# Kernel optimization log

Measured on AMD Instinct MI355X. Metric: run time of the kernel, lower is better.

The kernel has to match this reference:

```python
import jax, jax.numpy as jnp
import numpy as np

NUM_RADII, NUM_THETA = 3, 16
RADIUS = 40.0
DT = 0.1
RELU_SHIFT = 0.2
B, N, NB, T_ENC, OTHER_CH = 4, 512, 512, 16, 3


def _rot_mats():
    # bin-center angles of the num_theta angular bins
    t = (jnp.arange(NUM_THETA, dtype=jnp.float32) + 0.5) * (2.0 * jnp.pi / NUM_THETA) - jnp.pi
    c, s = jnp.cos(t), jnp.sin(t)
    return jnp.stack([jnp.stack([c, -s], -1), jnp.stack([s, c], -1)], -2)  # [T,2,2]


def _steer_kernel(W):
    # W: [R,T,O,I,2,2]; equivariant steering K[r,t] = R(theta_t) W[r,t] R(theta_t)^T
    Rm = _rot_mats()
    K = jnp.einsum('tab,rtoibc,tdc->rtoiad', Rm, W, Rm)
    return K.reshape(NUM_RADII * NUM_THETA, W.shape[2], W.shape[3], 2, 2)  # [K,O,I,2,2]


def _equi_conv(src_pos, qry_pos, feats, mask, W):
    # src_pos [B,S,2], qry_pos [B,Q,2], feats [B,S,I,2] vector features, mask [B,Q,S]
    rel = src_pos[:, None, :, :] - qry_pos[:, :, None, :]          # [B,Q,S,2]
    d2 = jnp.sum(rel * rel, -1)
    dist = jnp.sqrt(d2 + 1e-9)
    theta = jnp.arctan2(rel[..., 1], rel[..., 0])
    rb = jnp.clip((dist / RADIUS * NUM_RADII).astype(jnp.int32), 0, NUM_RADII - 1)
    tb = jnp.mod(jnp.floor((theta + jnp.pi) / (2.0 * jnp.pi) * NUM_THETA).astype(jnp.int32), NUM_THETA)
    kidx = rb * NUM_THETA + tb                                     # [B,Q,S] polar bin id
    win = jnp.maximum(1.0 - d2 / (RADIUS * RADIUS), 0.0) ** 3      # smooth radial window
    w = win * mask
    H = jax.nn.one_hot(kidx, NUM_RADII * NUM_THETA, dtype=feats.dtype) * w[..., None]  # [B,Q,S,K]
    M = jnp.einsum('bqsk,bsiv->bqkiv', H, feats)                   # bin-accumulated neighbor features
    K = _steer_kernel(W)
    return jnp.einsum('bqkiv,koiuv->bqou', M, K)                   # [B,Q,O,2]


def _equi_linear(f, A, Bm):
    # rotation-equivariant linear on vector channels: (a*I + b*J) per (out,in)
    Jf = jnp.stack([-f[..., 1], f[..., 0]], -1)
    return jnp.einsum('oi,bniv->bnov', A, f) + jnp.einsum('oi,bniv->bnov', Bm, Jf)


def _forward(p0_enc, v0_enc, p0, v0, a, other_feats, box, box_feats, fluid_mask, box_mask,
             W_cf, W_co, A_df, B_df, layer_params):
    # update_pos_vel
    v1 = v0 + DT * a
    p1 = p0 + DT * (v0 + v1) * 0.5
    # forward(): feats = cat(other_feats, v0_enc) on channel dim -2
    feats = jnp.concatenate([other_feats, v0_enc], -2)
    # compute_correction
    fluid_feats = jnp.concatenate([v1[:, :, None, :], feats], -2)  # [B,N,20,2]
    out_conv_fluid = _equi_conv(p1, p1, fluid_feats, fluid_mask, W_cf)
    out_dense_fluid = _equi_linear(fluid_feats, A_df, B_df)
    out_conv_obst = _equi_conv(box, p1, box_feats[:, :, None, :], box_mask, W_co)
    output = jnp.concatenate([out_conv_obst, out_conv_fluid, out_dense_fluid], -2)  # [B,N,48,2]
    for (Wc, Ad, Bd) in layer_params:
        mags = (jnp.sum(output * output, -1) + 1e-6)[..., None]
        in_feats = output / mags * jax.nn.relu(mags - RELU_SHIFT)
        oc = _equi_conv(p1, p1, in_feats, fluid_mask, Wc)
        od = _equi_linear(in_feats, Ad, Bd)
        if od.shape[-2] == output.shape[-2]:
            output = oc + od + output
        else:
            output = oc + od
    corr = output / 128.0                                          # [B,N,1,2]
    # apply_correction
    p_corrected = p1 + corr[..., 0, :]
    v_corrected = (p_corrected - p0) / DT
    return p_corrected, v_corrected


def setup_inputs():
    key = jax.random.key(0)
    ks = jax.random.split(key, 32)
    d = {}
    d['p0_enc'] = jax.random.normal(ks[0], (B, N, T_ENC, 2), jnp.float32)
    d['v0_enc'] = jax.random.normal(ks[1], (B, N, T_ENC, 2), jnp.float32)
    d['p0'] = jax.random.uniform(ks[2], (B, N, 2), jnp.float32) * 100.0
    d['v0'] = jax.random.normal(ks[3], (B, N, 2), jnp.float32)
    d['a'] = jax.random.normal(ks[4], (B, N, 2), jnp.float32)
    d['other_feats'] = jax.random.normal(ks[5], (B, N, OTHER_CH, 2), jnp.float32)
    d['box'] = jax.random.uniform(ks[6], (B, NB, 2), jnp.float32) * 100.0
    d['box_feats'] = jax.random.normal(ks[7], (B, NB, 2), jnp.float32)
    d['fluid_mask'] = (jax.random.uniform(ks[8], (B, N, N)) < 0.5).astype(jnp.float32)
    d['box_mask'] = (jax.random.uniform(ks[9], (B, N, NB)) < 0.5).astype(jnp.float32)
    sc = 0.05
    d['W_cf'] = sc * jax.random.normal(ks[10], (NUM_RADII, NUM_THETA, 16, 20, 2, 2), jnp.float32)
    d['W_co'] = sc * jax.random.normal(ks[11], (NUM_RADII, NUM_THETA, 16, 1, 2, 2), jnp.float32)
    d['A_df'] = sc * jax.random.normal(ks[12], (16, 20), jnp.float32)
    d['B_df'] = sc * jax.random.normal(ks[13], (16, 20), jnp.float32)
    chans = [(32, 48), (32, 32), (32, 32), (1, 32)]
    for i, (o, ci) in enumerate(chans, start=1):
        d['W_c%d' % i] = sc * jax.random.normal(ks[13 + 3 * i], (NUM_RADII, NUM_THETA, o, ci, 2, 2), jnp.float32)
        d['A_d%d' % i] = sc * jax.random.normal(ks[14 + 3 * i], (o, ci), jnp.float32)
        d['B_d%d' % i] = sc * jax.random.normal(ks[15 + 3 * i], (o, ci), jnp.float32)
    return d


def reference(p0_enc, v0_enc, p0, v0, a, other_feats, box, box_feats, fluid_mask, box_mask,
              W_cf, W_co, A_df, B_df, W_c1, A_d1, B_d1, W_c2, A_d2, B_d2,
              W_c3, A_d3, B_d3, W_c4, A_d4, B_d4):
    layer_params = [(W_c1, A_d1, B_d1), (W_c2, A_d2, B_d2), (W_c3, A_d3, B_d3), (W_c4, A_d4, B_d4)]
    return _forward(p0_enc, v0_enc, p0, v0, a, other_feats, box, box_feats, fluid_mask, box_mask,
                    W_cf, W_co, A_df, B_df, layer_params)
```

## Files before the change

### kernel.cpp

```cpp
#include <hip/hip_runtime.h>
#include <cstdint>
#include <cstddef>

#define PI_F 3.14159265358979323846f

constexpr int BB = 4, NN = 512, BN = 2048, NBIN = 48;

typedef __attribute__((ext_vector_type(8))) short v8s;
typedef __attribute__((ext_vector_type(4))) float v4f;

__device__ __forceinline__ unsigned short f2bf(float f) {
  unsigned u = __float_as_uint(f);
  unsigned r = (u + 0x7FFFu + ((u >> 16) & 1u)) >> 16;
  return (unsigned short)r;
}
__device__ __forceinline__ float bf2f(unsigned short s) {
  return __uint_as_float(((unsigned)s) << 16);
}

__device__ __forceinline__ void steer_f32(const float* __restrict__ W, float* __restrict__ K2,
                                          int O, int I, int Ipad, int idx, int total) {
  if (idx >= total) return;
  int i = idx % Ipad;
  int o = (idx / Ipad) % O;
  int k = idx / (Ipad * O);
  int CTc = O * 2;
  size_t r0 = (size_t)((k*Ipad + i)*2 + 0) * CTc + o*2;
  size_t r1 = r0 + CTc;
  if (i >= I) { K2[r0]=0.f; K2[r0+1]=0.f; K2[r1]=0.f; K2[r1+1]=0.f; return; }
  int tt = k % 16;
  float ang = (tt + 0.5f) * (2.0f * PI_F / 16.0f) - PI_F;
  float ct = cosf(ang), st = sinf(ang);
  const float* Wp = W + ((size_t)(k*O + o)*I + i) * 4;
  float w00 = Wp[0], w01 = Wp[1], w10 = Wp[2], w11 = Wp[3];
  float rw00 = ct*w00 - st*w10, rw01 = ct*w01 - st*w11;
  float rw10 = st*w00 + ct*w10, rw11 = st*w01 + ct*w11;
  K2[r0 + 0] = rw00*ct - rw01*st;
  K2[r0 + 1] = rw10*ct - rw11*st;
  K2[r1 + 0] = rw00*st + rw01*ct;
  K2[r1 + 1] = rw10*st + rw11*ct;
}

__device__ __forceinline__ void steer_bf16T(const float* __restrict__ W,
                                            unsigned short* __restrict__ K2T,
                                            int O, int I, int Ipad, int Kd,
                                            int idx, int total) {
  if (idx >= total) return;
  int i = idx % Ipad;
  int o = (idx / Ipad) % O;
  int k = idx / (Ipad * O);
  size_t c0 = (size_t)(o*2 + 0) * Kd + (k*Ipad + i)*2;
  size_t c1 = (size_t)(o*2 + 1) * Kd + (k*Ipad + i)*2;
  if (i >= I) { K2T[c0]=0; K2T[c0+1]=0; K2T[c1]=0; K2T[c1+1]=0; return; }
  int tt = k % 16;
  float ang = (tt + 0.5f) * (2.0f * PI_F / 16.0f) - PI_F;
  float ct = cosf(ang), st = sinf(ang);
  const float* Wp = W + ((size_t)(k*O + o)*I + i) * 4;
  float w00 = Wp[0], w01 = Wp[1], w10 = Wp[2], w11 = Wp[3];
  float rw00 = ct*w00 - st*w10, rw01 = ct*w01 - st*w11;
  float rw10 = st*w00 + ct*w10, rw11 = st*w01 + ct*w11;
  K2T[c0 + 0] = f2bf(rw00*ct - rw01*st);
  K2T[c0 + 1] = f2bf(rw00*st + rw01*ct);
  K2T[c1 + 0] = f2bf(rw10*ct - rw11*st);
  K2T[c1 + 1] = f2bf(rw10*st + rw11*ct);
}

__global__ __launch_bounds__(256) void setup_kernel(
    const float* __restrict__ p0, const float* __restrict__ v0,
    const float* __restrict__ a, const float* __restrict__ other,
    const float* __restrict__ v0enc, float* __restrict__ p1, float* __restrict__ F0,
    const float* Wcf, unsigned short* K2CF, const float* Wco, float* K2CO,
    const float* Wc1, unsigned short* K2C1, const float* Wc2, unsigned short* K2C2,
    const float* Wc3, unsigned short* K2C3, const float* Wc4, float* K2C4) {
  int blk = blockIdx.x;
  int t = threadIdx.x;
  if (blk < 8) {
    int n = blk * 256 + t;
    float p0x = p0[n*2], p0y = p0[n*2+1];
    float v0x = v0[n*2], v0y = v0[n*2+1];
    float ax = a[n*2],  ay = a[n*2+1];
    float v1x = v0x + 0.1f*ax, v1y = v0y + 0.1f*ay;
    p1[n*2]   = p0x + 0.1f*(v0x+v1x)*0.5f;
    p1[n*2+1] = p0y + 0.1f*(v0y+v1y)*0.5f;
    float* F = F0 + (size_t)n*48;
    F[0] = v1x; F[1] = v1y;
    for (int c = 0; c < 3; ++c) {
      F[2+c*2]   = other[(n*3+c)*2];
      F[2+c*2+1] = other[(n*3+c)*2+1];
    }
    for (int c = 0; c < 16; ++c) {
      F[8+c*2]   = v0enc[(n*16+c)*2];
      F[8+c*2+1] = v0enc[(n*16+c)*2+1];
    }
    for (int c = 40; c < 48; ++c) F[c] = 0.0f;
  } else if (blk < 80)  steer_bf16T(Wcf, K2CF, 16, 20, 24, 2304, (blk-8)*256 + t, 18432);
  else if (blk < 83)  steer_f32(Wco, K2CO, 16, 1, 1,   (blk-80)*256 + t, 768);
  else if (blk < 371) steer_bf16T(Wc1, K2C1, 32, 48, 48, 4608, (blk-83)*256 + t, 73728);
  else if (blk < 563) steer_bf16T(Wc2, K2C2, 32, 32, 32, 3072, (blk-371)*256 + t, 49152);
  else if (blk < 755) steer_bf16T(Wc3, K2C3, 32, 32, 32, 3072, (blk-563)*256 + t, 49152);
  else                steer_f32(Wc4, K2C4, 1, 32, 32,  (blk-755)*256 + t, 1536);
}

__global__ __launch_bounds__(256) void pairs_all(const float* __restrict__ qry,
                                                 const float* __restrict__ srcF,
                                                 const float* __restrict__ maskF,
                                                 float* __restrict__ wlF, int* __restrict__ plF,
                                                 int* __restrict__ cntF,
                                                 const float* __restrict__ srcO,
                                                 const float* __restrict__ maskO,
                                                 float* __restrict__ wlO, int* __restrict__ plO,
                                                 int* __restrict__ cntO) {
  __shared__ int hist[4][48];
  __shared__ int bstart[4][48];
  __shared__ int runc[4][48];
  bool isBox = blockIdx.x >= 512;
  int qblk = isBox ? (blockIdx.x - 512) : blockIdx.x;
  const float* src = isBox ? srcO : srcF;
  const float* mask = isBox ? maskO : maskF;
  float* wlist = isBox ? wlO : wlF;
  int* plist = isBox ? plO : plF;
  int* cnt = isBox ? cntO : cntF;

  int wv = threadIdx.x >> 6;
  int lane = threadIdx.x & 63;
  int q = qblk * 4 + wv;
  int b = q >> 9;
  float qx = qry[q*2], qy = qry[q*2+1];
  const float* sb = src + b*1024;
  const float* mb = mask + (size_t)q*512;
  float* wl = wlist + (size_t)q*512;
  int* pl = plist + (size_t)q*512;

  if (lane < 48) { hist[wv][lane] = 0; runc[wv][lane] = 0; }

  float wreg[8]; int kreg[8];
  unsigned char predreg[8];
  for (int ch = 0; ch < 8; ++ch) {
    int s = ch*64 + lane;
    float sx = sb[s*2], sy = sb[s*2+1];
    float rx = sx - qx, ry = sy - qy;
    float d2 = rx*rx + ry*ry;
    float m = mb[s];
    float wi = fmaxf(1.0f - d2 / 1600.0f, 0.0f);
    float w = wi*wi*wi*m;
    bool pred = w > 0.0f;
    int k = 63;
    if (pred) {
      float dist = sqrtf(d2 + 1e-9f);
      float theta = atan2f(ry, rx);
      int rb = (int)(dist / 40.0f * 3.0f);
      rb = rb > 2 ? 2 : rb;
      float u = (theta + PI_F) / (2.0f * PI_F) * 16.0f;
      int tb = ((int)floorf(u)) & 15;
      k = rb*16 + tb;
      atomicAdd(&hist[wv][k], 1);
    }
    wreg[ch] = w; kreg[ch] = k; predreg[ch] = pred ? 1 : 0;
  }
  int cntv = (lane < 48) ? hist[wv][lane] : 0;
  int sc = cntv;
  #pragma unroll
  for (int off = 1; off < 64; off <<= 1) {
    int o = __shfl_up(sc, off);
    if (lane >= off) sc += o;
  }
  if (lane < 48) bstart[wv][lane] = sc - cntv;
  if (lane == 47) cnt[q] = sc;

  for (int ch = 0; ch < 8; ++ch) {
    bool pred = predreg[ch] != 0;
    int k = kreg[ch];
    float w = wreg[ch];
    unsigned long long mEq = __ballot(pred);
    #pragma unroll
    for (int bit = 0; bit < 6; ++bit) {
      unsigned long long mbm = __ballot((k >> bit) & 1);
      mEq &= ((k >> bit) & 1) ? mbm : ~mbm;
    }
    int rank = __popcll(mEq & ((1ull<<lane)-1ull));
    int total = __popcll(mEq);
    if (pred) {
      int bs = bstart[wv][k];
      int rc = runc[wv][k];
      int pos = bs + rc + rank;
      int s = ch*64 + lane;
      wl[pos] = w;
      pl[pos] = (s<<6) | k;
      if (rank == total - 1) runc[wv][k] = rc + total;
    }
  }
}

__device__ __forceinline__ int find_split(const int* __restrict__ pls, int nnz) {
  if (nnz <= 0) return 0;
  int kmid = pls[nnz >> 1] & 63;
  int lo = nnz >> 1, hi = nnz;
  while (lo < hi) {
    int m2 = (lo + hi) >> 1;
    if ((pls[m2] & 63) > kmid) hi = m2; else lo = m2 + 1;
  }
  return lo;
}

template<int C2>
__device__ __forceinline__ void accum_range(float* __restrict__ M, int sw, int c,
    int jbeg, int jend,
    const float* __restrict__ wls, const int* __restrict__ pls,
    const float* __restrict__ fb) {
  int len = jend - jbeg;
  if (len <= 0) return;
  const float* wp = wls + jbeg;
  const int* pp = pls + jbeg;
  constexpr int W = 16;
  float wA[W], fA[W]; int kA[W];
  #pragma unroll
  for (int j = 0; j < W; ++j) {
    bool v = j < len;
    float wv = v ? wp[j] : 0.0f;
    int p = v ? pp[j] : 0;
    wA[j] = wv; kA[j] = v ? (p & 63) : NBIN;
    fA[j] = fb[(p >> 6) * C2];
  }
  int kcur = -1;
  float acc = 0.0f;
  for (int base = 0; base < len; base += W) {
    float wB[W], fB[W]; int kB[W];
    if (base + W < len) {
      #pragma unroll
      for (int j = 0; j < W; ++j) {
        int idx = base + W + j;
        bool v = idx < len;
        float wv = v ? wp[idx] : 0.0f;
        int p = v ? pp[idx] : 0;
        wB[j] = wv; kB[j] = v ? (p & 63) : NBIN;
        fB[j] = fb[(size_t)(p >> 6) * C2];
      }
    }
    asm volatile("" ::: "memory");
    #pragma unroll
    for (int j = 0; j < W; ++j) {
      acc = (kA[j] == kcur ? acc : 0.0f) + wA[j] * fA[j];
      kcur = kA[j];
      M[(kcur * C2 + c) ^ sw] = acc;
    }
    #pragma unroll
    for (int j = 0; j < W; ++j) { wA[j] = wB[j]; kA[j] = kB[j]; fA[j] = fB[j]; }
  }
}

template<int QB, int TPB>
__device__ __forceinline__ void stage_lists(int q0, const int* __restrict__ csh,
    const float* __restrict__ wlist, const int* __restrict__ plist,
    float* __restrict__ wsh, int* __restrict__ psh) {
  const int t = threadIdx.x;
  for (int i = t; i < QB*128; i += TPB) {
    int qs = i >> 7, j = i & 127;
    if (j*4 < csh[qs]) {
      ((float4*)(wsh + qs*512))[j] = ((const float4*)(wlist + (size_t)(q0+qs)*512))[j];
      ((int4*)(psh + qs*512))[j]   = ((const int4*)(plist + (size_t)(q0+qs)*512))[j];
    }
  }
}

template<int C2, int QB, int TPB>
__global__ __launch_bounds__(TPB, 1) void accum4(const float* __restrict__ wlist,
                                                 const int* __restrict__ plist,
                                                 const int* __restrict__ cnt,
                                                 const float* __restrict__ feats,
                                                 unsigned short* __restrict__ Mout) {
  constexpr int Kd = NBIN * C2;
  constexpr int KdP = Kd + C2;
  static_assert(TPB == 2 * QB * C2, "TPB must equal 2*QB*C2");
  __shared__ float Ml[QB * KdP];
  __shared__ float wsh[QB*512];
  __shared__ int   psh[QB*512];
  __shared__ int   csh[QB];
  const int t = threadIdx.x;
  const int q0 = blockIdx.x * QB;
  for (int i = t; i < QB*KdP; i += TPB) Ml[i] = 0.0f;
  if (t < QB) csh[t] = (q0 + t < BN) ? cnt[q0 + t] : 0;
  __syncthreads();
  stage_lists<QB, TPB>(q0, csh, wlist, plist, wsh, psh);
  __syncthreads();
  {
    const int ql = t / (2*C2);
    const int rem = t % (2*C2);
    const int half = rem / C2, c = rem % C2;
    const int q = q0 + ql;
    const int nnz = csh[ql];
    const int js = find_split(psh + ql*512, nnz);
    accum_range<C2>(Ml + ql*KdP, 0, c, half ? js : 0, half ? nnz : js,
                    wsh + ql*512, psh + ql*512,
                    feats + (size_t)(q >> 9)*512*C2 + c);
  }
  __syncthreads();
  for (int i = t; i < QB*(Kd/2); i += TPB) {
    int ql = i / (Kd/2), off = i % (Kd/2);
    float2 v = ((const float2*)(Ml + ql*KdP))[off];
    ((unsigned*)(Mout + (size_t)(q0+ql)*Kd))[off] =
        (unsigned)f2bf(v.x) | ((unsigned)f2bf(v.y) << 16);
  }
}

template<int CT>
__global__ __launch_bounds__(256) void gemm_mfma(const unsigned short* __restrict__ A,
                                                 const unsigned short* __restrict__ B,
                                                 float* __restrict__ G, int Kd, int kn) {
  const int lane = threadIdx.x & 63;
  const int w = threadIdx.x >> 6;
  const int mblk = blockIdx.x;
  const int ks = blockIdx.y * 4 + w;
  const int k0 = ks * kn;
  const int m = lane & 15, quad = lane >> 4;
  constexpr int NT = CT / 16;
  const unsigned short* Ar0 = A + (size_t)(mblk*32 + m) * Kd + k0 + quad*8;
  const unsigned short* Ar1 = Ar0 + (size_t)16 * Kd;
  const unsigned short* Bp[NT];
  #pragma unroll
  for (int nt = 0; nt < NT; ++nt)
    Bp[nt] = B + (size_t)(nt*16 + m) * Kd + k0 + quad*8;
  v4f acc[2][NT];
  #pragma unroll
  for (int mt = 0; mt < 2; ++mt)
    for (int nt = 0; nt < NT; ++nt)
      acc[mt][nt] = (v4f){0.0f, 0.0f, 0.0f, 0.0f};
  for (int kt = 0; kt < kn; kt += 32) {
    v8s a0 = *(const v8s*)(Ar0 + kt);
    v8s a1 = *(const v8s*)(Ar1 + kt);
    #pragma unroll
    for (int nt = 0; nt < NT; ++nt) {
      v8s bv = *(const v8s*)(Bp[nt] + kt);
      acc[0][nt] = __builtin_amdgcn_mfma_f32_16x16x32_bf16(a0, bv, acc[0][nt], 0, 0, 0);
      acc[1][nt] = __builtin_amdgcn_mfma_f32_16x16x32_bf16(a1, bv, acc[1][nt], 0, 0, 0);
    }
  }
  float* Gb = G + ((size_t)ks * BN + mblk*32) * CT;
  #pragma unroll
  for (int mt = 0; mt < 2; ++mt)
    for (int nt = 0; nt < NT; ++nt)
      for (int r = 0; r < 4; ++r)
        Gb[(mt*16 + quad*4 + r) * CT + nt*16 + m] = acc[mt][nt][r];
}

__global__ void epilogueL(const float* __restrict__ Gp, int SPLIT,
                          const float* __restrict__ inPrev, int I,
                          const float* __restrict__ Ad, const float* __restrict__ Bd,
                          const float* __restrict__ prevOut, int doRes,
                          float* __restrict__ outCur, float* __restrict__ inNext) {
  int idx = blockIdx.x * blockDim.x + threadIdx.x;
  if (idx >= BN*32) return;
  int o = idx % 32, q = idx / 32;
  float x = 0.0f, y = 0.0f;
  for (int sp = 0; sp < SPLIT; ++sp) {
    size_t base = ((size_t)sp*BN + q)*64 + o*2;
    x += Gp[base]; y += Gp[base+1];
  }
  const float* f = inPrev + (size_t)q * I * 2;
  for (int i = 0; i < I; ++i) {
    float fx = f[i*2], fy = f[i*2+1];
    float Av = Ad[o*I+i], Bv = Bd[o*I+i];
    x += Av*fx - Bv*fy;
    y += Av*fy + Bv*fx;
  }
  if (doRes) {
    x += prevOut[(size_t)idx*2];
    y += prevOut[(size_t)idx*2+1];
  }
  outCur[(size_t)idx*2]   = x;
  outCur[(size_t)idx*2+1] = y;
  float m = x*x + y*y + 1e-6f;
  float sc = fmaxf(m - 0.2f, 0.0f) / m;
  inNext[(size_t)idx*2]   = x * sc;
  inNext[(size_t)idx*2+1] = y * sc;
}

__global__ __launch_bounds__(512, 1) void fused_s0(
    const float* __restrict__ wlF, const int* __restrict__ plF, const int* __restrict__ cntF,
    const float* __restrict__ F0, const unsigned short* __restrict__ K2CF,
    const float* __restrict__ wlO, const int* __restrict__ plO, const int* __restrict__ cntO,
    const float* __restrict__ boxf, const float* __restrict__ K2CO,
    const float* __restrict__ Adf, const float* __restrict__ Bdf,
    float* __restrict__ in1) {
  constexpr int QB = 4;
  constexpr int Kd = 2304;
  constexpr int KdP = 2352;
  constexpr int NWv = 8;
  constexpr int KW = Kd / NWv;
  __shared__ float Ml[QB * KdP];
  __shared__ float Mo[QB * 98];
  __shared__ float red[NWv][QB * 32];
  __shared__ float wshF[QB*512];
  __shared__ int   pshF[QB*512];
  __shared__ float wshO[QB*512];
  __shared__ int   pshO[QB*512];
  __shared__ int cshF[QB];
  __shared__ int cshO[QB];
  const int t = threadIdx.x;
  const int q0 = blockIdx.x * QB;
  for (int i = t; i < QB*KdP; i += 512) Ml[i] = 0.0f;
  for (int i = t; i < QB*98; i += 512) Mo[i] = 0.0f;
  if (t < QB) cshF[t] = cntF[q0 + t];
  else if (t < 2*QB) cshO[t-QB] = cntO[q0 + t - QB];
  __syncthreads();
  for (int i = t; i < 2*QB*128; i += 512) {
    int half = i >> 9;
    int qs = (i >> 7) & (QB-1), j = i & 127;
    if (half == 0) {
      if (j*4 < cshF[qs]) {
        ((float4*)(wshF + qs*512))[j] = ((const float4*)(wlF + (size_t)(q0+qs)*512))[j];
        ((int4*)(pshF + qs*512))[j]   = ((const int4*)(plF + (size_t)(q0+qs)*512))[j];
      }
    } else {
      if (j*4 < cshO[qs]) {
        ((float4*)(wshO + qs*512))[j] = ((const float4*)(wlO + (size_t)(q0+qs)*512))[j];
        ((int4*)(pshO + qs*512))[j]   = ((const int4*)(plO + (size_t)(q0+qs)*512))[j];
      }
    }
  }
  __syncthreads();
  if (t < 384) {
    const int ql = t / 96, rem = t % 96;
    const int half = rem / 48, c = rem % 48;
    const int q = q0 + ql;
    const int nnz = cshF[ql];
    const int js = find_split(pshF + ql*512, nnz);
    accum_range<48>(Ml + ql*KdP, ql << 2, c, half ? js : 0, half ? nnz : js,
                    wshF + ql*512, pshF + ql*512,
                    F0 + (size_t)(q >> 9)*512*48 + c);
  } else if (t < 400) {
    const int idx = t - 384;
    const int ql = idx >> 2, half = (idx >> 1) & 1, c = idx & 1;
    const int q = q0 + ql;
    const int nnz = cshO[ql];
    const int js = find_split(pshO + ql*512, nnz);
    accum_range<2>(Mo + ql*98, 0, c, half ? js : 0, half ? nnz : js,
                   wshO + ql*512, pshO + ql*512,
                   boxf + (size_t)(q >> 9)*1024 + c);
  }
  __syncthreads();
  {
    const int lane = t & 63, w = t >> 6;
    const int m = lane & 15, quad = lane >> 4;
    const int ar = m & 3;
    const int sw = ar << 2;
    const float* Abase = Ml + ar * KdP;
    const int kb = w * KW + quad * 8;
    const unsigned short* Bb0 = K2CF + (size_t)m * Kd + kb;
    const unsigned short* Bb1 = K2CF + (size_t)(16 + m) * Kd + kb;
    v4f acc[2];
    acc[0] = (v4f){0,0,0,0}; acc[1] = (v4f){0,0,0,0};
    float4 a0c = *(const float4*)(Abase + (kb ^ sw));
    float4 a1c = *(const float4*)(Abase + ((kb + 4) ^ sw));
    v8s b0c = *(const v8s*)(Bb0);
    v8s b1c = *(const v8s*)(Bb1);
    for (int kt = 0; kt < KW; kt += 32) {
      float4 a0n, a1n; v8s b0n, b1n;
      if (kt + 32 < KW) {
        const int jn = kb + kt + 32;
        a0n = *(const float4*)(Abase + (jn ^ sw));
        a1n = *(const float4*)(Abase + ((jn + 4) ^ sw));
        b0n = *(const v8s*)(Bb0 + kt + 32);
        b1n = *(const v8s*)(Bb1 + kt + 32);
      }
      v8s av;
      av[0]=(short)f2bf(a0c.x); av[1]=(short)f2bf(a0c.y); av[2]=(short)f2bf(a0c.z); av[3]=(short)f2bf(a0c.w);
      av[4]=(short)f2bf(a1c.x); av[5]=(short)f2bf(a1c.y); av[6]=(short)f2bf(a1c.z); av[7]=(short)f2bf(a1c.w);
      acc[0] = __builtin_amdgcn_mfma_f32_16x16x32_bf16(av, b0c, acc[0], 0, 0, 0);
      acc[1] = __builtin_amdgcn_mfma_f32_16x16x32_bf16(av, b1c, acc[1], 0, 0, 0);
      a0c = a0n; a1c = a1n; b0c = b0n; b1c = b1n;
    }
    if (quad == 0) {
      #pragma unroll
      for (int nt = 0; nt < 2; ++nt)
        #pragma unroll
        for (int r = 0; r < 4; ++r)
          red[w][r*32 + nt*16 + m] = acc[nt][r];
    }
  }
  __syncthreads();
  if (t < 192) {
    const int ql = t / 48, ch = t % 48;
    const int q = q0 + ql;
    float x = 0.0f, y = 0.0f;
    if (ch < 16) {
      const float* Mq = Mo + ql*98;
      for (int j = 0; j < 96; ++j) {
        float mv = Mq[j];
        x += mv * K2CO[j*32 + ch*2];
        y += mv * K2CO[j*32 + ch*2 + 1];
      }
    } else if (ch < 32) {
      int o = ch - 16;
      #pragma unroll
      for (int w2 = 0; w2 < NWv; ++w2) {
        x += red[w2][ql*32 + o*2];
        y += red[w2][ql*32 + o*2 + 1];
      }
    } else {
      int o = ch - 32;
      const float* f = F0 + (size_t)q*48;
      for (int i = 0; i < 20; ++i) {
        float fx = f[i*2], fy = f[i*2+1];
        float Av = Adf[o*20+i], Bv = Bdf[o*20+i];
        x += Av*fx - Bv*fy;
        y += Av*fy + Bv*fx;
      }
    }
    float mm = x*x + y*y + 1e-6f;
    float sc = fmaxf(mm - 0.2f, 0.0f) / mm;
    size_t idx = (size_t)q*48 + ch;
    in1[idx*2]   = x * sc;
    in1[idx*2+1] = y * sc;
  }
}

template<int C2, int CT, int I, int QB>
__global__ __launch_bounds__(2*C2*QB, 1) void fused_layer(
    const float* __restrict__ wlist, const int* __restrict__ plist,
    const int* __restrict__ cnt, const float* __restrict__ feats,
    const unsigned short* __restrict__ K2T,
    const float* __restrict__ Ad, const float* __restrict__ Bd,
    const float* __restrict__ prevOut, int doRes,
    float* __restrict__ outCur, float* __restrict__ inNext) {
  constexpr int Kd = NBIN * C2;
  constexpr int KdP = Kd + C2;
  constexpr int TPB = 2 * C2 * QB;
  constexpr int NW = TPB / 64;
  constexpr int KW = Kd / NW;
  constexpr int NT = CT / 16;
  static_assert(KW % 32 == 0, "KW must be multiple of 32");
  __shared__ float Ml[QB * KdP];
  __shared__ float red[NW][QB * CT];
  __shared__ float wsh[QB*512];
  __shared__ int   psh[QB*512];
  __shared__ int csh[QB];
  const int t = threadIdx.x;
  const int q0 = blockIdx.x * QB;
  for (int i = t; i < QB*KdP; i += TPB) Ml[i] = 0.0f;
  if (t < QB) csh[t] = cnt[q0 + t];
  __syncthreads();
  stage_lists<QB, TPB>(q0, csh, wlist, plist, wsh, psh);
  __syncthreads();
  {
    const int ql = t / (2*C2);
    const int rem = t % (2*C2);
    const int half = rem / C2, c = rem % C2;
    const int q = q0 + ql;
    const int nnz = csh[ql];
    const int js = find_split(psh + ql*512, nnz);
    accum_range<C2>(Ml + ql*KdP, (ql & 3) << 2, c, half ? js : 0, half ? nnz : js,
                    wsh + ql*512, psh + ql*512,
                    feats + (size_t)(q >> 9)*512*C2 + c);
  }
  __syncthreads();
  const int lane = t & 63, w = t >> 6;
  const int m = lane & 15, quad = lane >> 4;
  const int ar = m & (QB-1);
  const int sw = ar << 2;
  const float* Abase = Ml + ar * KdP;
  const int kb = w * KW + quad * 8;
  const unsigned short* Bb[NT];
  #pragma unroll
  for (int nt = 0; nt < NT; ++nt)
    Bb[nt] = K2T + (size_t)(nt*16 + m) * Kd + kb;
  v4f acc[NT];
  #pragma unroll
  for (int nt = 0; nt < NT; ++nt) acc[nt] = (v4f){0,0,0,0};
  float4 a0c = *(const float4*)(Abase + (kb ^ sw));
  float4 a1c = *(const float4*)(Abase + ((kb + 4) ^ sw));
  v8s bc[NT];
  #pragma unroll
  for (int nt = 0; nt < NT; ++nt) bc[nt] = *(const v8s*)(Bb[nt]);
  for (int kt = 0; kt < KW; kt += 32) {
    float4 a0n, a1n; v8s bn[NT];
    if (kt + 32 < KW) {
      const int jn = kb + kt + 32;
      a0n = *(const float4*)(Abase + (jn ^ sw));
      a1n = *(const float4*)(Abase + ((jn + 4) ^ sw));
      #pragma unroll
      for (int nt = 0; nt < NT; ++nt) bn[nt] = *(const v8s*)(Bb[nt] + kt + 32);
    }
    v8s av;
    av[0]=(short)f2bf(a0c.x); av[1]=(short)f2bf(a0c.y); av[2]=(short)f2bf(a0c.z); av[3]=(short)f2bf(a0c.w);
    av[4]=(short)f2bf(a1c.x); av[5]=(short)f2bf(a1c.y); av[6]=(short)f2bf(a1c.z); av[7]=(short)f2bf(a1c.w);
    #pragma unroll
    for (int nt = 0; nt < NT; ++nt)
      acc[nt] = __builtin_amdgcn_mfma_f32_16x16x32_bf16(av, bc[nt], acc[nt], 0, 0, 0);
    a0c = a0n; a1c = a1n;
    #pragma unroll
    for (int nt = 0; nt < NT; ++nt) bc[nt] = bn[nt];
  }
  if (quad == 0) {
    #pragma unroll
    for (int nt = 0; nt < NT; ++nt)
      #pragma unroll
      for (int r = 0; r < QB; ++r)
        red[w][r*CT + nt*16 + m] = acc[nt][r];
  }
  __syncthreads();
  if (t < QB * (CT/2)) {
    const int o = t % (CT/2), ql = t / (CT/2);
    const int q = q0 + ql;
    float x = 0.0f, y = 0.0f;
    #pragma unroll
    for (int w2 = 0; w2 < NW; ++w2) {
      x += red[w2][ql*CT + o*2];
      y += red[w2][ql*CT + o*2 + 1];
    }
    const float* f = feats + (size_t)q * C2;
    for (int i = 0; i < I; ++i) {
      float fx = f[i*2], fy = f[i*2+1];
      float Av = Ad[o*I + i], Bv = Bd[o*I + i];
      x += Av*fx - Bv*fy;
      y += Av*fy + Bv*fx;
    }
    size_t idx = (size_t)q * (CT/2) + o;
    if (doRes) { x += prevOut[idx*2]; y += prevOut[idx*2+1]; }
    outCur[idx*2]   = x;
    outCur[idx*2+1] = y;
    float mm = x*x + y*y + 1e-6f;
    float sc = fmaxf(mm - 0.2f, 0.0f) / mm;
    inNext[idx*2]   = x * sc;
    inNext[idx*2+1] = y * sc;
  }
}

__global__ __launch_bounds__(512, 1) void fused_l4(
    const float* __restrict__ wl, const int* __restrict__ pl, const int* __restrict__ cnt,
    const float* __restrict__ in4, const float* __restrict__ K2C4,
    const float* __restrict__ Ad4, const float* __restrict__ Bd4,
    const float* __restrict__ p1, const float* __restrict__ p0,
    float* __restrict__ dout) {
  constexpr int QB = 4, Kd = 3072, KdP = 3136;
  __shared__ float Ml[QB * KdP];
  __shared__ float wsh[QB*512];
  __shared__ int   psh[QB*512];
  __shared__ int csh[QB];
  __shared__ float r4[QB][2][2];
  const int t = threadIdx.x;
  const int q0 = blockIdx.x * QB;
  for (int i = t; i < QB*KdP; i += 512) Ml[i] = 0.0f;
  if (t < QB) csh[t] = cnt[q0 + t];
  __syncthreads();
  stage_lists<QB, 512>(q0, csh, wl, pl, wsh, psh);
  __syncthreads();
  {
    const int ql = t / 128, rem = t % 128;
    const int half = rem / 64, c = rem % 64;
    const int q = q0 + ql;
    const int nnz = csh[ql];
    const int js = find_split(psh + ql*512, nnz);
    accum_range<64>(Ml + ql*KdP, (ql & 3) << 2, c, half ? js : 0, half ? nnz : js,
                    wsh + ql*512, psh + ql*512,
                    in4 + (size_t)(q >> 9)*512*64 + c);
  }
  __syncthreads();
  const int lane = t & 63, w = t >> 6;
  const int ql = w >> 1, kh = w & 1;
  const int q = q0 + ql;
  const int sw = ql << 2;
  const float* Mq = Ml + ql*KdP;
  float a0 = 0.0f, a1 = 0.0f;
  for (int j = kh*1536 + lane; j < kh*1536 + 1536; j += 64) {
    float av = Mq[j ^ sw];
    a0 += av * K2C4[j*2];
    a1 += av * K2C4[j*2+1];
  }
  if (kh == 0 && lane < 32) {
    float fx = in4[q*64 + lane*2], fy = in4[q*64 + lane*2 + 1];
    float Av = Ad4[lane], Bv = Bd4[lane];
    a0 += Av*fx - Bv*fy;
    a1 += Av*fy + Bv*fx;
  }
  for (int off = 32; off > 0; off >>= 1) {
    a0 += __shfl_down(a0, off);
    a1 += __shfl_down(a1, off);
  }
  if (lane == 0) { r4[ql][kh][0] = a0; r4[ql][kh][1] = a1; }
  __syncthreads();
  if (t < QB) {
    int qq = q0 + t;
    float s0 = r4[t][0][0] + r4[t][1][0];
    float s1 = r4[t][0][1] + r4[t][1][1];
    float px = p1[qq*2]   + s0/128.0f;
    float py = p1[qq*2+1] + s1/128.0f;
    dout[qq*2] = px; dout[qq*2+1] = py;
    dout[4096 + qq*2]   = (px - p0[qq*2]) / 0.1f;
    dout[4096 + qq*2+1] = (py - p0[qq*2+1]) / 0.1f;
  }
}

extern "C" void kernel_launch(void* const* d_in, const int* in_sizes, int n_in,
                              void* d_out, int out_size, void* d_ws, size_t ws_size,
                              hipStream_t stream) {
  (void)in_sizes; (void)n_in; (void)out_size; (void)ws_size;
  const float* v0_enc = (const float*)d_in[1];
  const float* p0     = (const float*)d_in[2];
  const float* v0     = (const float*)d_in[3];
  const float* a      = (const float*)d_in[4];
  const float* other  = (const float*)d_in[5];
  const float* box    = (const float*)d_in[6];
  const float* boxf   = (const float*)d_in[7];
  const float* fmask  = (const float*)d_in[8];
  const float* bmask  = (const float*)d_in[9];
  const float* Wcf = (const float*)d_in[10];
  const float* Wco = (const float*)d_in[11];
  const float* Adf = (const float*)d_in[12];
  const float* Bdf = (const float*)d_in[13];
  const float* Wc1 = (const float*)d_in[14];
  const float* Ad1 = (const float*)d_in[15];
  const float* Bd1 = (const float*)d_in[16];
  const float* Wc2 = (const float*)d_in[17];
  const float* Ad2 = (const float*)d_in[18];
  const float* Bd2 = (const float*)d_in[19];
  const float* Wc3 = (const float*)d_in[20];
  const float* Ad3 = (const float*)d_in[21];
  const float* Bd3 = (const float*)d_in[22];
  const float* Wc4 = (const float*)d_in[23];
  const float* Ad4 = (const float*)d_in[24];
  const float* Bd4 = (const float*)d_in[25];

  float* ws = (float*)d_ws;
  float* P1    = ws + 0;
  float* F0    = ws + 4096;
  unsigned short* K2CF = (unsigned short*)(ws + 102400);
  float* K2CO  = ws + 176128;
  unsigned short* K2C1 = (unsigned short*)(ws + 179200);
  unsigned short* K2C2 = (unsigned short*)(ws + 474112);
  unsigned short* K2C3 = (unsigned short*)(ws + 670720);
  float* K2C4  = ws + 867328;
  float* WFl   = ws + 873472;
  int*   PFl   = (int*)(ws + 1922048);
  int*   CNTF  = (int*)(ws + 2970624);
  int*   CNTO  = (int*)(ws + 2972672);
  float* IN1   = ws + 2974720;
  float* IN2   = ws + 3171328;
  float* IN3   = ws + 3302400;
  float* IN4   = ws + 3433472;
  float* OUTA  = ws + 3564544;
  float* OUTB  = ws + 3695616;
  float* GPART = ws + 4027392;
  unsigned short* MBUF = (unsigned short*)(ws + 6124544);
  float* WOl   = ws + 15561728;
  int*   POl   = (int*)(ws + 16610304);

  setup_kernel<<<761, 256, 0, stream>>>(p0, v0, a, other, v0_enc, P1, F0,
                                        Wcf, K2CF, Wco, K2CO, Wc1, K2C1,
                                        Wc2, K2C2, Wc3, K2C3, Wc4, K2C4);
  pairs_all<<<1024, 256, 0, stream>>>(P1, P1, fmask, WFl, PFl, CNTF,
                                      box, bmask, WOl, POl, CNTO);
  fused_s0<<<512, 512, 0, stream>>>(WFl, PFl, CNTF, F0, K2CF,
                                    WOl, POl, CNTO, boxf, K2CO, Adf, Bdf, IN1);
  accum4<96, 2, 384><<<1024, 384, 0, stream>>>(WFl, PFl, CNTF, IN1, MBUF);
  gemm_mfma<64><<<dim3(64, 4), 256, 0, stream>>>(MBUF, K2C1, GPART, 4608, 288);
  epilogueL<<<256, 256, 0, stream>>>(GPART, 16, IN1, 48, Ad1, Bd1, nullptr, 0, OUTA, IN2);
  fused_layer<64, 64, 32, 4><<<512, 512, 0, stream>>>(WFl, PFl, CNTF, IN2, K2C2,
                                                      Ad2, Bd2, OUTA, 1, OUTB, IN3);
  fused_layer<64, 64, 32, 4><<<512, 512, 0, stream>>>(WFl, PFl, CNTF, IN3, K2C3,
                                                      Ad3, Bd3, OUTB, 1, OUTA, IN4);
  fused_l4<<<512, 512, 0, stream>>>(WFl, PFl, CNTF, IN4, K2C4, Ad4, Bd4,
                                    P1, p0, (float*)d_out);
}
```

Baseline: 292.4 us.

## Merge setup and pair-building kernels; split neighbor accumulation into four segments

Setup and pair-list construction now run in one launch. The pair blocks recompute the updated positions inline instead of waiting on P1 from setup. The accum4 and fused_l4 kernels split each query's bin-sorted neighbor list into four segments instead of two, doubling threads per block, to get more parallelism in the accumulation. This removes one launch and a dependency, but recomputes positions redundantly and adds more segment boundaries, where threads working on the same bin may conflict.

```diff
diff --git a/kernel.cpp b/kernel.cpp
--- a/kernel.cpp
+++ b/kernel.cpp
@@ -65,15 +65,13 @@
   K2T[c1 + 1] = f2bf(rw10*st + rw11*ct);
 }
 
-__global__ __launch_bounds__(256) void setup_kernel(
+__device__ __forceinline__ void setup_body(int blk, int t,
     const float* __restrict__ p0, const float* __restrict__ v0,
     const float* __restrict__ a, const float* __restrict__ other,
     const float* __restrict__ v0enc, float* __restrict__ p1, float* __restrict__ F0,
     const float* Wcf, unsigned short* K2CF, const float* Wco, float* K2CO,
     const float* Wc1, unsigned short* K2C1, const float* Wc2, unsigned short* K2C2,
     const float* Wc3, unsigned short* K2C3, const float* Wc4, float* K2C4) {
-  int blk = blockIdx.x;
-  int t = threadIdx.x;
   if (blk < 8) {
     int n = blk * 256 + t;
     float p0x = p0[n*2], p0y = p0[n*2+1];
@@ -101,32 +99,42 @@
   else                steer_f32(Wc4, K2C4, 1, 32, 32,  (blk-755)*256 + t, 1536);
 }
 
-__global__ __launch_bounds__(256) void pairs_all(const float* __restrict__ qry,
-                                                 const float* __restrict__ srcF,
-                                                 const float* __restrict__ maskF,
-                                                 float* __restrict__ wlF, int* __restrict__ plF,
-                                                 int* __restrict__ cntF,
-                                                 const float* __restrict__ srcO,
-                                                 const float* __restrict__ maskO,
-                                                 float* __restrict__ wlO, int* __restrict__ plO,
-                                                 int* __restrict__ cntO) {
+__global__ __launch_bounds__(256) void setup_pairs(
+    const float* __restrict__ p0, const float* __restrict__ v0,
+    const float* __restrict__ a, const float* __restrict__ other,
+    const float* __restrict__ v0enc, float* __restrict__ P1, float* __restrict__ F0,
+    const float* Wcf, unsigned short* K2CF, const float* Wco, float* K2CO,
+    const float* Wc1, unsigned short* K2C1, const float* Wc2, unsigned short* K2C2,
+    const float* Wc3, unsigned short* K2C3, const float* Wc4, float* K2C4,
+    const float* __restrict__ maskF,
+    float* __restrict__ wlF, int* __restrict__ plF, int* __restrict__ cntF,
+    const float* __restrict__ box, const float* __restrict__ maskO,
+    float* __restrict__ wlO, int* __restrict__ plO, int* __restrict__ cntO) {
+  const int t = threadIdx.x;
+  if (blockIdx.x < 761) {
+    setup_body(blockIdx.x, t, p0, v0, a, other, v0enc, P1, F0,
+               Wcf, K2CF, Wco, K2CO, Wc1, K2C1, Wc2, K2C2, Wc3, K2C3, Wc4, K2C4);
+    return;
+  }
   __shared__ int hist[4][48];
   __shared__ int bstart[4][48];
   __shared__ int runc[4][48];
-  bool isBox = blockIdx.x >= 512;
-  int qblk = isBox ? (blockIdx.x - 512) : blockIdx.x;
-  const float* src = isBox ? srcO : srcF;
+  int pblk = blockIdx.x - 761;
+  bool isBox = pblk >= 512;
+  int qblk = isBox ? (pblk - 512) : pblk;
   const float* mask = isBox ? maskO : maskF;
   float* wlist = isBox ? wlO : wlF;
   int* plist = isBox ? plO : plF;
   int* cnt = isBox ? cntO : cntF;
 
-  int wv = threadIdx.x >> 6;
-  int lane = threadIdx.x & 63;
+  int wv = t >> 6;
+  int lane = t & 63;
   int q = qblk * 4 + wv;
   int b = q >> 9;
-  float qx = qry[q*2], qy = qry[q*2+1];
-  const float* sb = src + b*1024;
+  float qv1x = v0[q*2]   + 0.1f*a[q*2];
+  float qv1y = v0[q*2+1] + 0.1f*a[q*2+1];
+  float qx = p0[q*2]   + 0.1f*(v0[q*2]  +qv1x)*0.5f;
+  float qy = p0[q*2+1] + 0.1f*(v0[q*2+1]+qv1y)*0.5f;
   const float* mb = mask + (size_t)q*512;
   float* wl = wlist + (size_t)q*512;
   int* pl = plist + (size_t)q*512;
@@ -137,7 +145,16 @@
   unsigned char predreg[8];
   for (int ch = 0; ch < 8; ++ch) {
     int s = ch*64 + lane;
-    float sx = sb[s*2], sy = sb[s*2+1];
+    float sx, sy;
+    if (isBox) {
+      sx = box[(b*512+s)*2]; sy = box[(b*512+s)*2+1];
+    } else {
+      int n = b*512 + s;
+      float sv1x = v0[n*2]   + 0.1f*a[n*2];
+      float sv1y = v0[n*2+1] + 0.1f*a[n*2+1];
+      sx = p0[n*2]   + 0.1f*(v0[n*2]  +sv1x)*0.5f;
+      sy = p0[n*2+1] + 0.1f*(v0[n*2+1]+sv1y)*0.5f;
+    }
     float rx = sx - qx, ry = sy - qy;
     float d2 = rx*rx + ry*ry;
     float m = mb[s];
@@ -191,15 +208,18 @@
   }
 }
 
-__device__ __forceinline__ int find_split(const int* __restrict__ pls, int nnz) {
-  if (nnz <= 0) return 0;
-  int kmid = pls[nnz >> 1] & 63;
-  int lo = nnz >> 1, hi = nnz;
+__device__ __forceinline__ int find_split_at(const int* __restrict__ pls, int nnz, int target) {
+  if (target >= nnz) return nnz;
+  int kmid = pls[target] & 63;
+  int lo = target, hi = nnz;
   while (lo < hi) {
     int m2 = (lo + hi) >> 1;
     if ((pls[m2] & 63) > kmid) hi = m2; else lo = m2 + 1;
   }
   return lo;
+}
+__device__ __forceinline__ int find_split(const int* __restrict__ pls, int nnz) {
+  return find_split_at(pls, nnz, nnz >> 1);
 }
 
 template<int C2>
@@ -270,7 +290,7 @@
                                                  unsigned short* __restrict__ Mout) {
   constexpr int Kd = NBIN * C2;
   constexpr int KdP = Kd + C2;
-  static_assert(TPB == 2 * QB * C2, "TPB must equal 2*QB*C2");
+  static_assert(TPB == 4 * QB * C2, "TPB must equal 4*QB*C2");
   __shared__ float Ml[QB * KdP];
   __shared__ float wsh[QB*512];
   __shared__ int   psh[QB*512];
@@ -283,14 +303,16 @@
   stage_lists<QB, TPB>(q0, csh, wlist, plist, wsh, psh);
   __syncthreads();
   {
-    const int ql = t / (2*C2);
-    const int rem = t % (2*C2);
-    const int half = rem / C2, c = rem % C2;
+    const int ql = t / (4*C2);
+    const int rem = t % (4*C2);
+    const int seg = rem / C2, c = rem % C2;
     const int q = q0 + ql;
     const int nnz = csh[ql];
-    const int js = find_split(psh + ql*512, nnz);
-    accum_range<C2>(Ml + ql*KdP, 0, c, half ? js : 0, half ? nnz : js,
-                    wsh + ql*512, psh + ql*512,
+    const int* pls = psh + ql*512;
+    int b0 = (seg == 0) ? 0 : find_split_at(pls, nnz, (nnz*seg) >> 2);
+    int b1 = (seg == 3) ? nnz : find_split_at(pls, nnz, (nnz*(seg+1)) >> 2);
+    accum_range<C2>(Ml + ql*KdP, 0, c, b0, b1,
+                    wsh + ql*512, pls,
                     feats + (size_t)(q >> 9)*512*C2 + c);
   }
   __syncthreads();
@@ -625,7 +647,7 @@
   }
 }
 
-__global__ __launch_bounds__(512, 1) void fused_l4(
+__global__ __launch_bounds__(1024, 1) void fused_l4(
     const float* __restrict__ wl, const int* __restrict__ pl, const int* __restrict__ cnt,
     const float* __restrict__ in4, const float* __restrict__ K2C4,
     const float* __restrict__ Ad4, const float* __restrict__ Bd4,
@@ -636,37 +658,39 @@
   __shared__ float wsh[QB*512];
   __shared__ int   psh[QB*512];
   __shared__ int csh[QB];
-  __shared__ float r4[QB][2][2];
+  __shared__ float r4[QB][4][2];
   const int t = threadIdx.x;
   const int q0 = blockIdx.x * QB;
-  for (int i = t; i < QB*KdP; i += 512) Ml[i] = 0.0f;
+  for (int i = t; i < QB*KdP; i += 1024) Ml[i] = 0.0f;
   if (t < QB) csh[t] = cnt[q0 + t];
   __syncthreads();
-  stage_lists<QB, 512>(q0, csh, wl, pl, wsh, psh);
+  stage_lists<QB, 1024>(q0, csh, wl, pl, wsh, psh);
   __syncthreads();
   {
-    const int ql = t / 128, rem = t % 128;
-    const int half = rem / 64, c = rem % 64;
+    const int ql = t / 256, rem = t % 256;
+    const int seg = rem / 64, c = rem % 64;
     const int q = q0 + ql;
     const int nnz = csh[ql];
-    const int js = find_split(psh + ql*512, nnz);
-    accum_range<64>(Ml + ql*KdP, (ql & 3) << 2, c, half ? js : 0, half ? nnz : js,
-                    wsh + ql*512, psh + ql*512,
+    const int* pls = psh + ql*512;
+    int b0 = (seg == 0) ? 0 : find_split_at(pls, nnz, (nnz*seg) >> 2);
+    int b1 = (seg == 3) ? nnz : find_split_at(pls, nnz, (nnz*(seg+1)) >> 2);
+    accum_range<64>(Ml + ql*KdP, (ql & 3) << 2, c, b0, b1,
+                    wsh + ql*512, pls,
                     in4 + (size_t)(q >> 9)*512*64 + c);
   }
   __syncthreads();
   const int lane = t & 63, w = t >> 6;
-  const int ql = w >> 1, kh = w & 1;
+  const int ql = w >> 2, kq = w & 3;
   const int q = q0 + ql;
   const int sw = ql << 2;
   const float* Mq = Ml + ql*KdP;
   float a0 = 0.0f, a1 = 0.0f;
-  for (int j = kh*1536 + lane; j < kh*1536 + 1536; j += 64) {
+  for (int j = kq*768 + lane; j < kq*768 + 768; j += 64) {
     float av = Mq[j ^ sw];
     a0 += av * K2C4[j*2];
     a1 += av * K2C4[j*2+1];
   }
-  if (kh == 0 && lane < 32) {
+  if (kq == 0 && lane < 32) {
     float fx = in4[q*64 + lane*2], fy = in4[q*64 + lane*2 + 1];
     float Av = Ad4[lane], Bv = Bd4[lane];
     a0 += Av*fx - Bv*fy;
@@ -676,12 +700,12 @@
     a0 += __shfl_down(a0, off);
     a1 += __shfl_down(a1, off);
   }
-  if (lane == 0) { r4[ql][kh][0] = a0; r4[ql][kh][1] = a1; }
+  if (lane == 0) { r4[ql][kq][0] = a0; r4[ql][kq][1] = a1; }
   __syncthreads();
   if (t < QB) {
     int qq = q0 + t;
-    float s0 = r4[t][0][0] + r4[t][1][0];
-    float s1 = r4[t][0][1] + r4[t][1][1];
+    float s0 = r4[t][0][0] + r4[t][1][0] + r4[t][2][0] + r4[t][3][0];
+    float s1 = r4[t][0][1] + r4[t][1][1] + r4[t][2][1] + r4[t][3][1];
     float px = p1[qq*2]   + s0/128.0f;
     float py = p1[qq*2+1] + s1/128.0f;
     dout[qq*2] = px; dout[qq*2+1] = py;
@@ -744,20 +768,20 @@
   float* WOl   = ws + 15561728;
   int*   POl   = (int*)(ws + 16610304);
 
-  setup_kernel<<<761, 256, 0, stream>>>(p0, v0, a, other, v0_enc, P1, F0,
+  setup_pairs<<<1785, 256, 0, stream>>>(p0, v0, a, other, v0_enc, P1, F0,
                                         Wcf, K2CF, Wco, K2CO, Wc1, K2C1,
-                                        Wc2, K2C2, Wc3, K2C3, Wc4, K2C4);
-  pairs_all<<<1024, 256, 0, stream>>>(P1, P1, fmask, WFl, PFl, CNTF,
-                                      box, bmask, WOl, POl, CNTO);
+                                        Wc2, K2C2, Wc3, K2C3, Wc4, K2C4,
+                                        fmask, WFl, PFl, CNTF,
+                                        box, bmask, WOl, POl, CNTO);
   fused_s0<<<512, 512, 0, stream>>>(WFl, PFl, CNTF, F0, K2CF,
                                     WOl, POl, CNTO, boxf, K2CO, Adf, Bdf, IN1);
-  accum4<96, 2, 384><<<1024, 384, 0, stream>>>(WFl, PFl, CNTF, IN1, MBUF);
+  accum4<96, 2, 768><<<1024, 768, 0, stream>>>(WFl, PFl, CNTF, IN1, MBUF);
   gemm_mfma<64><<<dim3(64, 4), 256, 0, stream>>>(MBUF, K2C1, GPART, 4608, 288);
   epilogueL<<<256, 256, 0, stream>>>(GPART, 16, IN1, 48, Ad1, Bd1, nullptr, 0, OUTA, IN2);
   fused_layer<64, 64, 32, 4><<<512, 512, 0, stream>>>(WFl, PFl, CNTF, IN2, K2C2,
                                                       Ad2, Bd2, OUTA, 1, OUTB, IN3);
   fused_layer<64, 64, 32, 4><<<512, 512, 0, stream>>>(WFl, PFl, CNTF, IN3, K2C3,
                                                       Ad3, Bd3, OUTB, 1, OUTA, IN4);
-  fused_l4<<<512, 512, 0, stream>>>(WFl, PFl, CNTF, IN4, K2C4, Ad4, Bd4,
-                                    P1, p0, (float*)d_out);
-}
+  fused_l4<<<512, 1024, 0, stream>>>(WFl, PFl, CNTF, IN4, K2C4, Ad4, Bd4,
+                                     P1, p0, (float*)d_out);
+}
```

Result: no change. 294.7 us (+0.8%).
